# Optimization experiments

Measured on AMD Instinct MI355X. Metric: run time of the kernel, lower is better.

## Reference

```python
import jax, jax.numpy as jnp
from jax import lax
import numpy as np

N = 8192
STEPS = 128
CLAMP = 0.999


def setup_inputs() -> dict:
    key = jax.random.key(0)
    kz, kK = jax.random.split(key)
    z = jax.random.normal(kz, (N, 2), dtype=jnp.float32)
    K = jax.random.normal(kK, (N, N), dtype=jnp.float32) * 0.1
    omega = jnp.float32(0.1)
    dt = jnp.float32(0.01)
    return {"z": z, "K": K, "omega": omega, "dt": dt, "steps": STEPS}


def reference(z, K, omega, dt, steps):
    n = K.shape[0]
    inv2n = 1.0 / (2.0 * n)
    Kc = K.astype(jnp.complex64)  # K is real; imag part is zero
    zc = lax.complex(z[:, 0], z[:, 1])  # [N] complex64

    def step(zc, _):
        S = Kc @ jnp.conj(zc)                      # [N] complex GEMV
        t1 = (-inv2n) * S * (zc * zc)
        t2 = omega * zc
        t3 = inv2n * (Kc @ zc)
        zc = zc + dt * (t1 + t2 + t3)
        absz = jnp.abs(zc)
        mask = absz >= CLAMP
        safe = jnp.where(mask, absz, jnp.float32(1.0))
        zc = jnp.where(mask, zc / safe * CLAMP, zc)
        return zc, None

    zc, _ = lax.scan(step, zc, None, length=steps)
    z_f = jnp.stack([jnp.real(zc), jnp.imag(zc)], axis=-1)  # [N, 2]
    norms = jnp.linalg.norm(z_f, axis=1, keepdims=True)
    mask = norms >= CLAMP
    safe = jnp.where(mask, norms, jnp.float32(1.0))
    return jnp.where(mask, z_f / safe * CLAMP, z_f)
```

## Files before the change

### kernel.cpp

```cpp
#include <hip/hip_runtime.h>

#define NN 8192
#define STEPS 128
#define CLAMP_V 0.999f
#define WPR 1024
#define NBLK 256
#define TPB 1024

typedef unsigned long long ull;

#if __has_builtin(__builtin_amdgcn_sdot4)
#define DOT4(a, b, c) __builtin_amdgcn_sdot4((int)(a), (int)(b), (c), false)
#else
__device__ __forceinline__ int dot4_fb(int a, int b, int c) {
#pragma unroll
  for (int i = 0; i < 4; ++i)
    c += ((int)(signed char)(a >> (8 * i))) * ((int)(signed char)(b >> (8 * i)));
  return c;
}
#define DOT4(a, b, c) dot4_fb((int)(a), (int)(b), (c))
#endif

#if __has_builtin(__builtin_amdgcn_perm)
#define PERM(a, b, s) __builtin_amdgcn_perm((a), (b), (s))
#else
__device__ __forceinline__ unsigned perm_fb(unsigned a, unsigned b, unsigned s) {
  unsigned long long v = ((unsigned long long)a << 32) | b;
  unsigned r = 0;
#pragma unroll
  for (int i = 0; i < 4; ++i) r |= ((unsigned)(v >> (8 * ((s >> (8 * i)) & 7))) & 0xFF) << (8 * i);
  return r;
}
#define PERM(a, b, s) perm_fb((a), (b), (s))
#endif

__global__ __launch_bounds__(256) void quant4_kernel(const float* __restrict__ K,
                                                     unsigned* __restrict__ Kq,
                                                     float* __restrict__ scales) {
  const int row = blockIdx.x;
  const int tid = threadIdx.x;
  const int wave = tid >> 6, lane = tid & 63;
  const size_t base = (size_t)row * NN;

  float4 va[4], vb[4];
  float mx = 0.f;
#pragma unroll
  for (int g = 0; g < 4; ++g) {
    const size_t o = base + (size_t)(g * 256 + tid) * 8;
    va[g] = *(const float4*)(K + o);
    vb[g] = *(const float4*)(K + o + 4);
    mx = fmaxf(mx, fmaxf(fmaxf(fabsf(va[g].x), fabsf(va[g].y)),
                         fmaxf(fabsf(va[g].z), fabsf(va[g].w))));
    mx = fmaxf(mx, fmaxf(fmaxf(fabsf(vb[g].x), fabsf(vb[g].y)),
                         fmaxf(fabsf(vb[g].z), fabsf(vb[g].w))));
  }
#pragma unroll
  for (int off = 32; off > 0; off >>= 1) mx = fmaxf(mx, __shfl_xor(mx, off));
  __shared__ float wm[4];
  if (lane == 0) wm[wave] = mx;
  __syncthreads();
  mx = fmaxf(fmaxf(wm[0], wm[1]), fmaxf(wm[2], wm[3]));

  const float inv = (mx > 0.f) ? 7.f / mx : 0.f;
  if (tid == 0) scales[row] = mx / 112.f;

  const int b = row >> 5, wv = (row & 31) >> 1, ab = row & 1;

#pragma unroll
  for (int g = 0; g < 4; ++g) {
    int qa[4], qb[4];
    const float a4[4] = {va[g].x, va[g].y, va[g].z, va[g].w};
    const float b4[4] = {vb[g].x, vb[g].y, vb[g].z, vb[g].w};
#pragma unroll
    for (int i = 0; i < 4; ++i) {
      qa[i] = max(-7, min(7, __float2int_rn(a4[i] * inv)));
      qb[i] = max(-7, min(7, __float2int_rn(b4[i] * inv)));
    }
    unsigned w = 0;
#pragma unroll
    for (int i = 0; i < 4; ++i) {
      w |= ((unsigned)(qa[i] & 0xF)) << (8 * i);
      w |= ((unsigned)(qb[i] & 0xF)) << (8 * i + 4);
    }
    const int widx = g * 256 + tid;
    const int seg = widx >> 6, l = widx & 63;
    Kq[(size_t)((b * 16 + wv) * 64 + l) * 32 + ab * 16 + seg] = w;
  }
}

__global__ __launch_bounds__(256) void prep_kernel(const float* __restrict__ z,
                                                   ull* __restrict__ tz0,
                                                   ull* __restrict__ tz1,
                                                   float* __restrict__ scz) {
  const int tid = threadIdx.x;
  const int wave = tid >> 6, lane = tid & 63;
  float4 buf[16];
  float mx = 0.f;
#pragma unroll
  for (int j = 0; j < 16; ++j) {
    buf[j] = *(const float4*)(z + tid * 64 + j * 4);
    mx = fmaxf(mx, fmaxf(fmaxf(fabsf(buf[j].x), fabsf(buf[j].y)),
                         fmaxf(fabsf(buf[j].z), fabsf(buf[j].w))));
  }
#pragma unroll
  for (int off = 32; off > 0; off >>= 1) mx = fmaxf(mx, __shfl_xor(mx, off));
  __shared__ float wm[4];
  if (lane == 0) wm[wave] = mx;
  __syncthreads();
  mx = fmaxf(fmaxf(wm[0], wm[1]), fmaxf(wm[2], wm[3]));
  const float q = (mx > 0.f) ? 127.f / mx : 0.f;
  if (tid == 0) scz[0] = mx / 127.f;
#pragma unroll
  for (int j = 0; j < 16; ++j) {
    const int p = tid * 16 + j;
    const unsigned a = (unsigned)(max(-127, min(127, __float2int_rn(buf[j].x * q)))) & 0xFFu;
    const unsigned b = (unsigned)(max(-127, min(127, __float2int_rn(buf[j].y * q)))) & 0xFFu;
    const unsigned c = (unsigned)(max(-127, min(127, __float2int_rn(buf[j].z * q)))) & 0xFFu;
    const unsigned d = (unsigned)(max(-127, min(127, __float2int_rn(buf[j].w * q)))) & 0xFFu;
    tz0[p] = (ull)(a | (b << 8) | (c << 16) | (d << 24));
    tz1[p] = 0xFFFFFFFFull << 32;
  }
}

__global__ __launch_bounds__(TPB, 4)
void persist_kernel(const unsigned* __restrict__ Kq, const float* __restrict__ scales,
                    const float* __restrict__ z_in,
                    ull* __restrict__ tz0, ull* __restrict__ tz1,
                    const float* __restrict__ scz_p,
                    const float* __restrict__ omega_p, const float* __restrict__ dt_p,
                    float* __restrict__ out) {
  const int tid = threadIdx.x;
  const int wave = tid >> 6, lane = tid & 63;
  const int rowA = blockIdx.x * 32 + wave * 2;
  const int pair = blockIdx.x * 16 + wave;

  __shared__ ull lds_re[1024];
  __shared__ ull lds_im[1024];

  const int isB = lane & 1;
  float zr_s = z_in[2 * rowA + 2 * isB];
  float zi_s = z_in[2 * rowA + 2 * isB + 1];
  const float mySc = scales[rowA + isB];
  const float omega = *omega_p, dt = *dt_p;
  const float inv2n = 1.0f / (2.0f * (float)NN);
  const float sz0 = *scz_p;

  const int j = wave * 64 + lane;
  const uint4* kp = (const uint4*)(Kq + (size_t)((blockIdx.x * 16 + wave) * 64 + lane) * 32);

  for (int s = 0; s < STEPS; ++s) {
    const ull* tzc = (s & 1) ? tz1 : tz0;
    const unsigned tagw = (unsigned)s;

    uint4 kv[8];
#pragma unroll
    for (int r = 0; r < 8; ++r) kv[r] = kp[r];

    ull t0 = 0, t1 = 0, t2 = 0, t3 = 0;
    {
      const ull* p4 = tzc + 4 * j;
      bool k0 = false, k1 = false, k2 = false, k3 = false;
      for (;;) {
        if (!k0) { t0 = __hip_atomic_load(p4 + 0, __ATOMIC_RELAXED, __HIP_MEMORY_SCOPE_AGENT);
                   k0 = ((unsigned)(t0 >> 32) == tagw); }
        if (!k1) { t1 = __hip_atomic_load(p4 + 1, __ATOMIC_RELAXED, __HIP_MEMORY_SCOPE_AGENT);
                   k1 = ((unsigned)(t1 >> 32) == tagw); }
        if (!k2) { t2 = __hip_atomic_load(p4 + 2, __ATOMIC_RELAXED, __HIP_MEMORY_SCOPE_AGENT);
                   k2 = ((unsigned)(t2 >> 32) == tagw); }
        if (!k3) { t3 = __hip_atomic_load(p4 + 3, __ATOMIC_RELAXED, __HIP_MEMORY_SCOPE_AGENT);
                   k3 = ((unsigned)(t3 >> 32) == tagw); }
        if (__all(k0 && k1 && k2 && k3)) break;
        __builtin_amdgcn_s_sleep(1);
      }
    }
    {
      const unsigned lo0 = (unsigned)t0, lo1 = (unsigned)t1;
      const unsigned lo2 = (unsigned)t2, lo3 = (unsigned)t3;
      const unsigned re0123 = PERM(lo1, lo0, 0x06040200u);
      const unsigned re4567 = PERM(lo3, lo2, 0x06040200u);
      const unsigned im0123 = PERM(lo1, lo0, 0x07050301u);
      const unsigned im4567 = PERM(lo3, lo2, 0x07050301u);
      lds_re[j] = (ull)re0123 | ((ull)re4567 << 32);
      lds_im[j] = (ull)im0123 | ((ull)im4567 << 32);
    }
    __syncthreads();

    int srA = 0, siA = 0, srB = 0, siB = 0;
#pragma unroll
    for (int seg = 0; seg < 16; ++seg) {
      const ull zr = lds_re[seg * 64 + lane];
      const ull zi = lds_im[seg * 64 + lane];
      const unsigned zrl = (unsigned)zr, zrh = (unsigned)(zr >> 32);
      const unsigned zil = (unsigned)zi, zih = (unsigned)(zi >> 32);
      const uint4 ka4 = kv[seg >> 2];
      const uint4 kb4 = kv[4 + (seg >> 2)];
      const unsigned wA = (seg & 3) == 0 ? ka4.x : (seg & 3) == 1 ? ka4.y
                        : (seg & 3) == 2 ? ka4.z : ka4.w;
      const unsigned wB = (seg & 3) == 0 ? kb4.x : (seg & 3) == 1 ? kb4.y
                        : (seg & 3) == 2 ? kb4.z : kb4.w;
      const unsigned loA = (wA << 4) & 0xF0F0F0F0u, hiA = wA & 0xF0F0F0F0u;
      const unsigned loB = (wB << 4) & 0xF0F0F0F0u, hiB = wB & 0xF0F0F0F0u;
      srA = DOT4(loA, zrl, srA); srA = DOT4(hiA, zrh, srA);
      siA = DOT4(loA, zil, siA); siA = DOT4(hiA, zih, siA);
      srB = DOT4(loB, zrl, srB); srB = DOT4(hiB, zrh, srB);
      siB = DOT4(loB, zil, siB); siB = DOT4(hiB, zih, siB);
    }

#pragma unroll
    for (int off = 32; off > 0; off >>= 1) {
      srA += __shfl_xor(srA, off); siA += __shfl_xor(siA, off);
      srB += __shfl_xor(srB, off); siB += __shfl_xor(siB, off);
    }

    const int sr = isB ? srB : srA;
    const int si = isB ? siB : siA;
    const float sz = (s == 0) ? sz0 : (1.f / 127.f);
    const float fac = mySc * sz;
    const float Wr = (float)sr * fac, Wi = (float)si * fac;
    const float z2r = zr_s * zr_s - zi_s * zi_s;
    const float z2i = 2.0f * zr_s * zi_s;
    const float t1r = -inv2n * (Wr * z2r + Wi * z2i);
    const float t1i = -inv2n * (Wr * z2i - Wi * z2r);
    float nr = zr_s + dt * (t1r + omega * zr_s + inv2n * Wr);
    float ni = zi_s + dt * (t1i + omega * zi_s + inv2n * Wi);
    const float a = sqrtf(nr * nr + ni * ni);
    if (a >= CLAMP_V) { nr = nr / a * CLAMP_V; ni = ni / a * CLAMP_V; }
    zr_s = nr; zi_s = ni;

    if (s == STEPS - 1) {
      float fr = nr, fi = ni;
      const float n2 = sqrtf(fr * fr + fi * fi);
      if (n2 >= CLAMP_V) { fr = fr / n2 * CLAMP_V; fi = fi / n2 * CLAMP_V; }
      const float frB = __shfl(fr, 1);
      const float fiB = __shfl(fi, 1);
      if (lane == 0) {
        float4 o; o.x = fr; o.y = fi; o.z = frB; o.w = fiB;
        *(float4*)(out + 2 * rowA) = o;
      }
    } else {
      const unsigned pr = (unsigned)__float2int_rn(nr * 127.f) & 0xFFu;
      const unsigned pi = (unsigned)__float2int_rn(ni * 127.f) & 0xFFu;
      const unsigned half = pr | (pi << 8);
      const unsigned other = __shfl_xor(half, 1);
      if (lane == 0) {
        const ull w = (ull)(half | (other << 16)) | ((ull)(unsigned)(s + 1) << 32);
        __hip_atomic_store(((s & 1) ? tz0 : tz1) + pair, w,
                           __ATOMIC_RELAXED, __HIP_MEMORY_SCOPE_AGENT);
      }
    }
    __syncthreads();
  }
}

__global__ __launch_bounds__(256, 2)
void step_f32(const float* __restrict__ K,
              const float* __restrict__ z_old, float* __restrict__ z_new,
              const float* __restrict__ omega_p, const float* __restrict__ dt_p) {
  const int tid = threadIdx.x;
  const int wave = tid >> 6, lane = tid & 63;
  const int row0 = blockIdx.x * 8;
  __shared__ float red[4][16];
  float ar[8] = {0, 0, 0, 0, 0, 0, 0, 0};
  float ai[8] = {0, 0, 0, 0, 0, 0, 0, 0};
  const int cbase = wave * 2048 + lane * 8;
#pragma unroll
  for (int it = 0; it < 4; ++it) {
    const int c = cbase + it * 512;
    const float4 zA = *(const float4*)(z_old + 2 * c + 0);
    const float4 zB = *(const float4*)(z_old + 2 * c + 4);
    const float4 zC = *(const float4*)(z_old + 2 * c + 8);
    const float4 zD = *(const float4*)(z_old + 2 * c + 12);
#pragma unroll
    for (int r = 0; r < 8; ++r) {
      const float* kp = K + (size_t)(row0 + r) * NN + c;
      const float4 ka = *(const float4*)kp;
      const float4 kb = *(const float4*)(kp + 4);
      float sr = ar[r], si = ai[r];
      sr = fmaf(ka.x, zA.x, sr); si = fmaf(ka.x, zA.y, si);
      sr = fmaf(ka.y, zA.z, sr); si = fmaf(ka.y, zA.w, si);
      sr = fmaf(ka.z, zB.x, sr); si = fmaf(ka.z, zB.y, si);
      sr = fmaf(ka.w, zB.z, sr); si = fmaf(ka.w, zB.w, si);
      sr = fmaf(kb.x, zC.x, sr); si = fmaf(kb.x, zC.y, si);
      sr = fmaf(kb.y, zC.z, sr); si = fmaf(kb.y, zC.w, si);
      sr = fmaf(kb.z, zD.x, sr); si = fmaf(kb.z, zD.y, si);
      sr = fmaf(kb.w, zD.z, sr); si = fmaf(kb.w, zD.w, si);
      ar[r] = sr; ai[r] = si;
    }
  }
#pragma unroll
  for (int off = 32; off > 0; off >>= 1) {
#pragma unroll
    for (int r = 0; r < 8; ++r) {
      ar[r] += __shfl_xor(ar[r], off);
      ai[r] += __shfl_xor(ai[r], off);
    }
  }
  if (lane == 0) {
#pragma unroll
    for (int r = 0; r < 8; ++r) {
      red[wave][2 * r + 0] = ar[r];
      red[wave][2 * r + 1] = ai[r];
    }
  }
  __syncthreads();
  if (tid < 8) {
    const float Wr = red[0][2 * tid] + red[1][2 * tid] + red[2][2 * tid] + red[3][2 * tid];
    const float Wi = red[0][2 * tid + 1] + red[1][2 * tid + 1] +
                     red[2][2 * tid + 1] + red[3][2 * tid + 1];
    const int row = row0 + tid;
    const float omega = *omega_p;
    const float dt = *dt_p;
    const float inv2n = 1.0f / (2.0f * (float)NN);
    const float zr = z_old[2 * row];
    const float zi = z_old[2 * row + 1];
    const float z2r = zr * zr - zi * zi;
    const float z2i = 2.0f * zr * zi;
    const float t1r = -inv2n * (Wr * z2r + Wi * z2i);
    const float t1i = -inv2n * (Wr * z2i - Wi * z2r);
    float nr = zr + dt * (t1r + omega * zr + inv2n * Wr);
    float ni = zi + dt * (t1i + omega * zi + inv2n * Wi);
    const float a = sqrtf(nr * nr + ni * ni);
    if (a >= CLAMP_V) { nr = nr / a * CLAMP_V; ni = ni / a * CLAMP_V; }
    z_new[2 * row] = nr;
    z_new[2 * row + 1] = ni;
  }
}

__global__ __launch_bounds__(256) void finalize_kernel(const float* __restrict__ z,
                                                       float* __restrict__ out) {
  int i = blockIdx.x * blockDim.x + threadIdx.x;
  if (i < NN) {
    float x = z[2 * i], y = z[2 * i + 1];
    float n = sqrtf(x * x + y * y);
    if (n >= CLAMP_V) { x = x / n * CLAMP_V; y = y / n * CLAMP_V; }
    out[2 * i] = x;
    out[2 * i + 1] = y;
  }
}

extern "C" void kernel_launch(void* const* d_in, const int* in_sizes, int n_in,
                              void* d_out, int out_size, void* d_ws, size_t ws_size,
                              hipStream_t stream) {
  const float* z_in = (const float*)d_in[0];
  const float* K = (const float*)d_in[1];
  const float* omega_p = (const float*)d_in[2];
  const float* dt_p = (const float*)d_in[3];
  float* out = (float*)d_out;

  char* ws = (char*)d_ws;
  const size_t kq_bytes = (size_t)NN * WPR * sizeof(unsigned);
  const size_t sc_bytes = (size_t)NN * sizeof(float);
  const size_t tz_bytes = (size_t)(NN / 2) * sizeof(ull);
  const size_t need = kq_bytes + sc_bytes + 2 * tz_bytes + 256;

  if (ws_size >= need) {
    size_t off = 0;
    unsigned* Kq = (unsigned*)(ws + off); off += kq_bytes;
    float* scales = (float*)(ws + off); off += sc_bytes;
    ull* tz0 = (ull*)(ws + off); off += tz_bytes;
    ull* tz1 = (ull*)(ws + off); off += tz_bytes;
    float* scz = (float*)(ws + off);

    quant4_kernel<<<NN, 256, 0, stream>>>(K, Kq, scales);
    prep_kernel<<<1, 256, 0, stream>>>(z_in, tz0, tz1, scz);
    persist_kernel<<<NBLK, TPB, 0, stream>>>(Kq, scales, z_in, tz0, tz1,
                                             scz, omega_p, dt_p, out);
  } else {
    float* zb0 = (float*)ws;
    float* zb1 = zb0 + NN * 2;
    const float* src = z_in;
    for (int s = 0; s < STEPS; ++s) {
      float* dst = (s & 1) ? zb1 : zb0;
      step_f32<<<NN / 8, 256, 0, stream>>>(K, src, dst, omega_p, dt_p);
      src = dst;
    }
    finalize_kernel<<<(NN + 255) / 256, 256, 0, stream>>>(src, out);
  }
}
```

Measured before the change: 743.8 us.

## Replace block barriers with per-wave LDS flags and double-buffered z tiles

Both __syncthreads in the persistent step loop are removed. Waves now publish their decoded z segment into a double-buffered LDS tile and set a per-wave flag; consumers spin only on the four flags of the segment group they need next. The K quantization layout is rotated so each wave group begins with a different segment group, which staggers LDS traffic and lets waves start computing before the whole block arrives. The aim is to cut block-wide barrier stalls, at the cost of LDS spin polling and a more fragile ordering argument, since double buffering alone has to stop buffer reuse two steps later.

```diff
diff --git a/kernel.cpp b/kernel.cpp
--- a/kernel.cpp
+++ b/kernel.cpp
@@ -84,7 +84,8 @@
     }
     const int widx = g * 256 + tid;
     const int seg = widx >> 6, l = widx & 63;
-    Kq[(size_t)((b * 16 + wv) * 64 + l) * 32 + ab * 16 + seg] = w;
+    const int kpos = ((((seg >> 2) - (wv >> 2)) & 3) << 2) | (seg & 3);
+    Kq[(size_t)((b * 16 + wv) * 64 + l) * 32 + ab * 16 + kpos] = w;
   }
 }
 
@@ -134,8 +135,11 @@
   const int rowA = blockIdx.x * 32 + wave * 2;
   const int pair = blockIdx.x * 16 + wave;
 
-  __shared__ ull lds_re[1024];
-  __shared__ ull lds_im[1024];
+  __shared__ ull lds_re[2][1024];
+  __shared__ ull lds_im[2][1024];
+  __shared__ int sflag[16];
+  if (tid < 16) sflag[tid] = -1;
+  __syncthreads();
 
   const int isB = lane & 1;
   float zr_s = z_in[2 * rowA + 2 * isB];
@@ -146,11 +150,13 @@
   const float sz0 = *scz_p;
 
   const int j = wave * 64 + lane;
+  const int wg = wave >> 2;
   const uint4* kp = (const uint4*)(Kq + (size_t)((blockIdx.x * 16 + wave) * 64 + lane) * 32);
 
   for (int s = 0; s < STEPS; ++s) {
     const ull* tzc = (s & 1) ? tz1 : tz0;
     const unsigned tagw = (unsigned)s;
+    const int buf = s & 1;
 
     uint4 kv[8];
 #pragma unroll
@@ -180,30 +186,46 @@
       const unsigned re4567 = PERM(lo3, lo2, 0x06040200u);
       const unsigned im0123 = PERM(lo1, lo0, 0x07050301u);
       const unsigned im4567 = PERM(lo3, lo2, 0x07050301u);
-      lds_re[j] = (ull)re0123 | ((ull)re4567 << 32);
-      lds_im[j] = (ull)im0123 | ((ull)im4567 << 32);
-    }
-    __syncthreads();
+      lds_re[buf][j] = (ull)re0123 | ((ull)re4567 << 32);
+      lds_im[buf][j] = (ull)im0123 | ((ull)im4567 << 32);
+    }
+    if (lane == 0)
+      __hip_atomic_store(&sflag[wave], s, __ATOMIC_RELEASE, __HIP_MEMORY_SCOPE_WORKGROUP);
 
     int srA = 0, siA = 0, srB = 0, siB = 0;
 #pragma unroll
-    for (int seg = 0; seg < 16; ++seg) {
-      const ull zr = lds_re[seg * 64 + lane];
-      const ull zi = lds_im[seg * 64 + lane];
-      const unsigned zrl = (unsigned)zr, zrh = (unsigned)(zr >> 32);
-      const unsigned zil = (unsigned)zi, zih = (unsigned)(zi >> 32);
-      const uint4 ka4 = kv[seg >> 2];
-      const uint4 kb4 = kv[4 + (seg >> 2)];
-      const unsigned wA = (seg & 3) == 0 ? ka4.x : (seg & 3) == 1 ? ka4.y
-                        : (seg & 3) == 2 ? ka4.z : ka4.w;
-      const unsigned wB = (seg & 3) == 0 ? kb4.x : (seg & 3) == 1 ? kb4.y
-                        : (seg & 3) == 2 ? kb4.z : kb4.w;
-      const unsigned loA = (wA << 4) & 0xF0F0F0F0u, hiA = wA & 0xF0F0F0F0u;
-      const unsigned loB = (wB << 4) & 0xF0F0F0F0u, hiB = wB & 0xF0F0F0F0u;
-      srA = DOT4(loA, zrl, srA); srA = DOT4(hiA, zrh, srA);
-      siA = DOT4(loA, zil, siA); siA = DOT4(hiA, zih, siA);
-      srB = DOT4(loB, zrl, srB); srB = DOT4(hiB, zrh, srB);
-      siB = DOT4(loB, zil, siB); siB = DOT4(hiB, zih, siB);
+    for (int m = 0; m < 4; ++m) {
+      const int grp = (wg + m) & 3;
+      for (;;) {
+        const int f0 = __hip_atomic_load(&sflag[4 * grp + 0], __ATOMIC_ACQUIRE,
+                                         __HIP_MEMORY_SCOPE_WORKGROUP);
+        const int f1 = __hip_atomic_load(&sflag[4 * grp + 1], __ATOMIC_ACQUIRE,
+                                         __HIP_MEMORY_SCOPE_WORKGROUP);
+        const int f2 = __hip_atomic_load(&sflag[4 * grp + 2], __ATOMIC_ACQUIRE,
+                                         __HIP_MEMORY_SCOPE_WORKGROUP);
+        const int f3 = __hip_atomic_load(&sflag[4 * grp + 3], __ATOMIC_ACQUIRE,
+                                         __HIP_MEMORY_SCOPE_WORKGROUP);
+        if (min(min(f0, f1), min(f2, f3)) >= s) break;
+        __builtin_amdgcn_s_sleep(1);
+      }
+#pragma unroll
+      for (int t = 0; t < 4; ++t) {
+        const int seg = 4 * grp + t;
+        const ull zr = lds_re[buf][seg * 64 + lane];
+        const ull zi = lds_im[buf][seg * 64 + lane];
+        const unsigned zrl = (unsigned)zr, zrh = (unsigned)(zr >> 32);
+        const unsigned zil = (unsigned)zi, zih = (unsigned)(zi >> 32);
+        const unsigned wA = (t == 0) ? kv[m].x : (t == 1) ? kv[m].y
+                          : (t == 2) ? kv[m].z : kv[m].w;
+        const unsigned wB = (t == 0) ? kv[4 + m].x : (t == 1) ? kv[4 + m].y
+                          : (t == 2) ? kv[4 + m].z : kv[4 + m].w;
+        const unsigned loA = (wA << 4) & 0xF0F0F0F0u, hiA = wA & 0xF0F0F0F0u;
+        const unsigned loB = (wB << 4) & 0xF0F0F0F0u, hiB = wB & 0xF0F0F0F0u;
+        srA = DOT4(loA, zrl, srA); srA = DOT4(hiA, zrh, srA);
+        siA = DOT4(loA, zil, siA); siA = DOT4(hiA, zih, siA);
+        srB = DOT4(loB, zrl, srB); srB = DOT4(hiB, zrh, srB);
+        siB = DOT4(loB, zil, siB); siB = DOT4(hiB, zih, siB);
+      }
     }
 
 #pragma unroll
@@ -248,7 +270,6 @@
                            __ATOMIC_RELAXED, __HIP_MEMORY_SCOPE_AGENT);
       }
     }
-    __syncthreads();
   }
 }
 
```

After: 1.476 ms. 98.4% more time.

## Delegate global z polling to two stager waves with LDS flags and double buffer

Applied to the files above, without the earlier changes.

Only waves 14 and 15 now poll the global tagged z buffer and unpack it into a double-buffered LDS copy. They then publish a workgroup-scope flag, and the other waves spin on that flag instead of using __syncthreads. The trailing barrier is dropped because the LDS buffer alternates each step. The aim is to cut global polling traffic and barrier cost, at the price of serializing the unpacking onto two waves and adding LDS flag spinning.

```diff
diff --git a/kernel.cpp b/kernel.cpp
--- a/kernel.cpp
+++ b/kernel.cpp
@@ -134,8 +134,11 @@
   const int rowA = blockIdx.x * 32 + wave * 2;
   const int pair = blockIdx.x * 16 + wave;
 
-  __shared__ ull lds_re[1024];
-  __shared__ ull lds_im[1024];
+  __shared__ ull lds_re[2][1024];
+  __shared__ ull lds_im[2][1024];
+  __shared__ int sflag[2];
+  if (tid < 2) sflag[tid] = -1;
+  __syncthreads();
 
   const int isB = lane & 1;
   float zr_s = z_in[2 * rowA + 2 * isB];
@@ -145,51 +148,67 @@
   const float inv2n = 1.0f / (2.0f * (float)NN);
   const float sz0 = *scz_p;
 
-  const int j = wave * 64 + lane;
+  const bool stager = (wave >= 14);
+  const int sk = wave - 14;
   const uint4* kp = (const uint4*)(Kq + (size_t)((blockIdx.x * 16 + wave) * 64 + lane) * 32);
 
   for (int s = 0; s < STEPS; ++s) {
     const ull* tzc = (s & 1) ? tz1 : tz0;
     const unsigned tagw = (unsigned)s;
+    const int buf = s & 1;
 
     uint4 kv[8];
 #pragma unroll
     for (int r = 0; r < 8; ++r) kv[r] = kp[r];
 
-    ull t0 = 0, t1 = 0, t2 = 0, t3 = 0;
-    {
-      const ull* p4 = tzc + 4 * j;
-      bool k0 = false, k1 = false, k2 = false, k3 = false;
+    if (stager) {
+      bool kd[8] = {false, false, false, false, false, false, false, false};
       for (;;) {
-        if (!k0) { t0 = __hip_atomic_load(p4 + 0, __ATOMIC_RELAXED, __HIP_MEMORY_SCOPE_AGENT);
-                   k0 = ((unsigned)(t0 >> 32) == tagw); }
-        if (!k1) { t1 = __hip_atomic_load(p4 + 1, __ATOMIC_RELAXED, __HIP_MEMORY_SCOPE_AGENT);
-                   k1 = ((unsigned)(t1 >> 32) == tagw); }
-        if (!k2) { t2 = __hip_atomic_load(p4 + 2, __ATOMIC_RELAXED, __HIP_MEMORY_SCOPE_AGENT);
-                   k2 = ((unsigned)(t2 >> 32) == tagw); }
-        if (!k3) { t3 = __hip_atomic_load(p4 + 3, __ATOMIC_RELAXED, __HIP_MEMORY_SCOPE_AGENT);
-                   k3 = ((unsigned)(t3 >> 32) == tagw); }
-        if (__all(k0 && k1 && k2 && k3)) break;
+        bool allk = true;
+#pragma unroll
+        for (int r = 0; r < 8; ++r) {
+          if (!kd[r]) {
+            const int j = sk * 512 + r * 64 + lane;
+            const ull* p4 = tzc + 4 * j;
+            const ull t0 = __hip_atomic_load(p4 + 0, __ATOMIC_RELAXED, __HIP_MEMORY_SCOPE_AGENT);
+            const ull t1 = __hip_atomic_load(p4 + 1, __ATOMIC_RELAXED, __HIP_MEMORY_SCOPE_AGENT);
+            const ull t2 = __hip_atomic_load(p4 + 2, __ATOMIC_RELAXED, __HIP_MEMORY_SCOPE_AGENT);
+            const ull t3 = __hip_atomic_load(p4 + 3, __ATOMIC_RELAXED, __HIP_MEMORY_SCOPE_AGENT);
+            if (((unsigned)(t0 >> 32) == tagw) && ((unsigned)(t1 >> 32) == tagw) &&
+                ((unsigned)(t2 >> 32) == tagw) && ((unsigned)(t3 >> 32) == tagw)) {
+              const unsigned lo0 = (unsigned)t0, lo1 = (unsigned)t1;
+              const unsigned lo2 = (unsigned)t2, lo3 = (unsigned)t3;
+              const unsigned re0123 = PERM(lo1, lo0, 0x06040200u);
+              const unsigned re4567 = PERM(lo3, lo2, 0x06040200u);
+              const unsigned im0123 = PERM(lo1, lo0, 0x07050301u);
+              const unsigned im4567 = PERM(lo3, lo2, 0x07050301u);
+              lds_re[buf][j] = (ull)re0123 | ((ull)re4567 << 32);
+              lds_im[buf][j] = (ull)im0123 | ((ull)im4567 << 32);
+              kd[r] = true;
+            } else {
+              allk = false;
+            }
+          }
+        }
+        if (__all(allk)) break;
         __builtin_amdgcn_s_sleep(1);
       }
-    }
-    {
-      const unsigned lo0 = (unsigned)t0, lo1 = (unsigned)t1;
-      const unsigned lo2 = (unsigned)t2, lo3 = (unsigned)t3;
-      const unsigned re0123 = PERM(lo1, lo0, 0x06040200u);
-      const unsigned re4567 = PERM(lo3, lo2, 0x06040200u);
-      const unsigned im0123 = PERM(lo1, lo0, 0x07050301u);
-      const unsigned im4567 = PERM(lo3, lo2, 0x07050301u);
-      lds_re[j] = (ull)re0123 | ((ull)re4567 << 32);
-      lds_im[j] = (ull)im0123 | ((ull)im4567 << 32);
-    }
-    __syncthreads();
+      if (lane == 0)
+        __hip_atomic_store(&sflag[sk], s, __ATOMIC_RELEASE, __HIP_MEMORY_SCOPE_WORKGROUP);
+    }
+
+    for (;;) {
+      const int f0 = __hip_atomic_load(&sflag[0], __ATOMIC_ACQUIRE, __HIP_MEMORY_SCOPE_WORKGROUP);
+      const int f1 = __hip_atomic_load(&sflag[1], __ATOMIC_ACQUIRE, __HIP_MEMORY_SCOPE_WORKGROUP);
+      if (min(f0, f1) >= s) break;
+      __builtin_amdgcn_s_sleep(1);
+    }
 
     int srA = 0, siA = 0, srB = 0, siB = 0;
 #pragma unroll
     for (int seg = 0; seg < 16; ++seg) {
-      const ull zr = lds_re[seg * 64 + lane];
-      const ull zi = lds_im[seg * 64 + lane];
+      const ull zr = lds_re[buf][seg * 64 + lane];
+      const ull zi = lds_im[buf][seg * 64 + lane];
       const unsigned zrl = (unsigned)zr, zrh = (unsigned)(zr >> 32);
       const unsigned zil = (unsigned)zi, zih = (unsigned)(zi >> 32);
       const uint4 ka4 = kv[seg >> 2];
@@ -248,7 +267,6 @@
                            __ATOMIC_RELAXED, __HIP_MEMORY_SCOPE_AGENT);
       }
     }
-    __syncthreads();
   }
 }
 
```

Measured after the change: 1.074 ms. +44.3%, slower.

## Replace per-element tagged polling with per-block flags and one polling wave

Applied to the files above, without the earlier changes.

Replaces the inter-block handoff, which tagged every packed z word with a step number and had all 1024 threads poll global memory, with separate data buffers plus one release-flag per block. Only wave 15 polls the 256 flags and signals the rest of the block through a shared-memory variable. Each block collects its 16 packed outputs in LDS and has a few lanes publish them together before setting its flag. This cuts global polling traffic and halves the size of the z buffers, at the cost of an extra hop through the flag and a serial intra-block signal. It also relies on relaxed data stores being ordered before the release flag and made visible to readers.

```diff
diff --git a/kernel.cpp b/kernel.cpp
--- a/kernel.cpp
+++ b/kernel.cpp
@@ -89,8 +89,8 @@
 }
 
 __global__ __launch_bounds__(256) void prep_kernel(const float* __restrict__ z,
-                                                   ull* __restrict__ tz0,
-                                                   ull* __restrict__ tz1,
+                                                   unsigned* __restrict__ pz0,
+                                                   int* __restrict__ flags,
                                                    float* __restrict__ scz) {
   const int tid = threadIdx.x;
   const int wave = tid >> 6, lane = tid & 63;
@@ -110,6 +110,7 @@
   mx = fmaxf(fmaxf(wm[0], wm[1]), fmaxf(wm[2], wm[3]));
   const float q = (mx > 0.f) ? 127.f / mx : 0.f;
   if (tid == 0) scz[0] = mx / 127.f;
+  flags[tid] = 0;
 #pragma unroll
   for (int j = 0; j < 16; ++j) {
     const int p = tid * 16 + j;
@@ -117,25 +118,28 @@
     const unsigned b = (unsigned)(max(-127, min(127, __float2int_rn(buf[j].y * q)))) & 0xFFu;
     const unsigned c = (unsigned)(max(-127, min(127, __float2int_rn(buf[j].z * q)))) & 0xFFu;
     const unsigned d = (unsigned)(max(-127, min(127, __float2int_rn(buf[j].w * q)))) & 0xFFu;
-    tz0[p] = (ull)(a | (b << 8) | (c << 16) | (d << 24));
-    tz1[p] = 0xFFFFFFFFull << 32;
+    pz0[p] = a | (b << 8) | (c << 16) | (d << 24);
   }
 }
 
 __global__ __launch_bounds__(TPB, 4)
 void persist_kernel(const unsigned* __restrict__ Kq, const float* __restrict__ scales,
                     const float* __restrict__ z_in,
-                    ull* __restrict__ tz0, ull* __restrict__ tz1,
+                    unsigned* __restrict__ pz0, unsigned* __restrict__ pz1,
+                    int* __restrict__ flags,
                     const float* __restrict__ scz_p,
                     const float* __restrict__ omega_p, const float* __restrict__ dt_p,
                     float* __restrict__ out) {
   const int tid = threadIdx.x;
   const int wave = tid >> 6, lane = tid & 63;
   const int rowA = blockIdx.x * 32 + wave * 2;
-  const int pair = blockIdx.x * 16 + wave;
-
-  __shared__ ull lds_re[1024];
-  __shared__ ull lds_im[1024];
+
+  __shared__ ull lds_re[2][1024];
+  __shared__ ull lds_im[2][1024];
+  __shared__ unsigned pub[16];
+  __shared__ int gflag;
+  if (tid == 0) gflag = -1;
+  __syncthreads();
 
   const int isB = lane & 1;
   float zr_s = z_in[2 * rowA + 2 * isB];
@@ -145,51 +149,57 @@
   const float inv2n = 1.0f / (2.0f * (float)NN);
   const float sz0 = *scz_p;
 
-  const int j = wave * 64 + lane;
   const uint4* kp = (const uint4*)(Kq + (size_t)((blockIdx.x * 16 + wave) * 64 + lane) * 32);
 
   for (int s = 0; s < STEPS; ++s) {
-    const ull* tzc = (s & 1) ? tz1 : tz0;
-    const unsigned tagw = (unsigned)s;
+    const int buf = s & 1;
 
     uint4 kv[8];
 #pragma unroll
     for (int r = 0; r < 8; ++r) kv[r] = kp[r];
 
-    ull t0 = 0, t1 = 0, t2 = 0, t3 = 0;
-    {
-      const ull* p4 = tzc + 4 * j;
+    if (wave == 15) {
       bool k0 = false, k1 = false, k2 = false, k3 = false;
       for (;;) {
-        if (!k0) { t0 = __hip_atomic_load(p4 + 0, __ATOMIC_RELAXED, __HIP_MEMORY_SCOPE_AGENT);
-                   k0 = ((unsigned)(t0 >> 32) == tagw); }
-        if (!k1) { t1 = __hip_atomic_load(p4 + 1, __ATOMIC_RELAXED, __HIP_MEMORY_SCOPE_AGENT);
-                   k1 = ((unsigned)(t1 >> 32) == tagw); }
-        if (!k2) { t2 = __hip_atomic_load(p4 + 2, __ATOMIC_RELAXED, __HIP_MEMORY_SCOPE_AGENT);
-                   k2 = ((unsigned)(t2 >> 32) == tagw); }
-        if (!k3) { t3 = __hip_atomic_load(p4 + 3, __ATOMIC_RELAXED, __HIP_MEMORY_SCOPE_AGENT);
-                   k3 = ((unsigned)(t3 >> 32) == tagw); }
+        if (!k0) k0 = __hip_atomic_load(&flags[lane], __ATOMIC_RELAXED,
+                                        __HIP_MEMORY_SCOPE_AGENT) >= s;
+        if (!k1) k1 = __hip_atomic_load(&flags[lane + 64], __ATOMIC_RELAXED,
+                                        __HIP_MEMORY_SCOPE_AGENT) >= s;
+        if (!k2) k2 = __hip_atomic_load(&flags[lane + 128], __ATOMIC_RELAXED,
+                                        __HIP_MEMORY_SCOPE_AGENT) >= s;
+        if (!k3) k3 = __hip_atomic_load(&flags[lane + 192], __ATOMIC_RELAXED,
+                                        __HIP_MEMORY_SCOPE_AGENT) >= s;
         if (__all(k0 && k1 && k2 && k3)) break;
         __builtin_amdgcn_s_sleep(1);
       }
-    }
+      if (lane == 0)
+        __hip_atomic_store(&gflag, s, __ATOMIC_RELEASE, __HIP_MEMORY_SCOPE_WORKGROUP);
+    }
+    while (__hip_atomic_load(&gflag, __ATOMIC_ACQUIRE, __HIP_MEMORY_SCOPE_WORKGROUP) < s)
+      __builtin_amdgcn_s_sleep(1);
+
     {
-      const unsigned lo0 = (unsigned)t0, lo1 = (unsigned)t1;
-      const unsigned lo2 = (unsigned)t2, lo3 = (unsigned)t3;
+      const ull* pzc = (const ull*)((s & 1) ? pz1 : pz0);
+      const ull t0 = __hip_atomic_load(&pzc[2 * tid], __ATOMIC_RELAXED,
+                                       __HIP_MEMORY_SCOPE_AGENT);
+      const ull t1 = __hip_atomic_load(&pzc[2 * tid + 1], __ATOMIC_RELAXED,
+                                       __HIP_MEMORY_SCOPE_AGENT);
+      const unsigned lo0 = (unsigned)t0, lo1 = (unsigned)(t0 >> 32);
+      const unsigned lo2 = (unsigned)t1, lo3 = (unsigned)(t1 >> 32);
       const unsigned re0123 = PERM(lo1, lo0, 0x06040200u);
       const unsigned re4567 = PERM(lo3, lo2, 0x06040200u);
       const unsigned im0123 = PERM(lo1, lo0, 0x07050301u);
       const unsigned im4567 = PERM(lo3, lo2, 0x07050301u);
-      lds_re[j] = (ull)re0123 | ((ull)re4567 << 32);
-      lds_im[j] = (ull)im0123 | ((ull)im4567 << 32);
+      lds_re[buf][tid] = (ull)re0123 | ((ull)re4567 << 32);
+      lds_im[buf][tid] = (ull)im0123 | ((ull)im4567 << 32);
     }
     __syncthreads();
 
     int srA = 0, siA = 0, srB = 0, siB = 0;
 #pragma unroll
     for (int seg = 0; seg < 16; ++seg) {
-      const ull zr = lds_re[seg * 64 + lane];
-      const ull zi = lds_im[seg * 64 + lane];
+      const ull zr = lds_re[buf][seg * 64 + lane];
+      const ull zi = lds_im[buf][seg * 64 + lane];
       const unsigned zrl = (unsigned)zr, zrh = (unsigned)(zr >> 32);
       const unsigned zil = (unsigned)zi, zih = (unsigned)(zi >> 32);
       const uint4 ka4 = kv[seg >> 2];
@@ -242,13 +252,18 @@
       const unsigned pi = (unsigned)__float2int_rn(ni * 127.f) & 0xFFu;
       const unsigned half = pr | (pi << 8);
       const unsigned other = __shfl_xor(half, 1);
-      if (lane == 0) {
-        const ull w = (ull)(half | (other << 16)) | ((ull)(unsigned)(s + 1) << 32);
-        __hip_atomic_store(((s & 1) ? tz0 : tz1) + pair, w,
-                           __ATOMIC_RELAXED, __HIP_MEMORY_SCOPE_AGENT);
-      }
+      if (lane == 0) pub[wave] = half | (other << 16);
     }
     __syncthreads();
+
+    if (s < STEPS - 1 && wave == 0 && lane < 16) {
+      unsigned* pzn = (s & 1) ? pz0 : pz1;
+      __hip_atomic_store(&pzn[16 * blockIdx.x + lane], pub[lane],
+                         __ATOMIC_RELAXED, __HIP_MEMORY_SCOPE_AGENT);
+      if (lane == 0)
+        __hip_atomic_store(&flags[blockIdx.x], s + 1,
+                           __ATOMIC_RELEASE, __HIP_MEMORY_SCOPE_AGENT);
+    }
   }
 }
 
@@ -350,20 +365,22 @@
   char* ws = (char*)d_ws;
   const size_t kq_bytes = (size_t)NN * WPR * sizeof(unsigned);
   const size_t sc_bytes = (size_t)NN * sizeof(float);
-  const size_t tz_bytes = (size_t)(NN / 2) * sizeof(ull);
-  const size_t need = kq_bytes + sc_bytes + 2 * tz_bytes + 256;
+  const size_t pz_bytes = (size_t)(NN / 2) * sizeof(unsigned);
+  const size_t fl_bytes = (size_t)NBLK * sizeof(int);
+  const size_t need = kq_bytes + sc_bytes + 2 * pz_bytes + fl_bytes + 256;
 
   if (ws_size >= need) {
     size_t off = 0;
     unsigned* Kq = (unsigned*)(ws + off); off += kq_bytes;
     float* scales = (float*)(ws + off); off += sc_bytes;
-    ull* tz0 = (ull*)(ws + off); off += tz_bytes;
-    ull* tz1 = (ull*)(ws + off); off += tz_bytes;
+    unsigned* pz0 = (unsigned*)(ws + off); off += pz_bytes;
+    unsigned* pz1 = (unsigned*)(ws + off); off += pz_bytes;
+    int* flags = (int*)(ws + off); off += fl_bytes;
     float* scz = (float*)(ws + off);
 
     quant4_kernel<<<NN, 256, 0, stream>>>(K, Kq, scales);
-    prep_kernel<<<1, 256, 0, stream>>>(z_in, tz0, tz1, scz);
-    persist_kernel<<<NBLK, TPB, 0, stream>>>(Kq, scales, z_in, tz0, tz1,
+    prep_kernel<<<1, 256, 0, stream>>>(z_in, pz0, flags, scz);
+    persist_kernel<<<NBLK, TPB, 0, stream>>>(Kq, scales, z_in, pz0, pz1, flags,
                                              scz, omega_p, dt_p, out);
   } else {
     float* zb0 = (float*)ws;
```

Result: slower. 1.211 ms (+62.8%).
